# Optimization experiments

Hardware: AMD Instinct MI355X
Metric: run time of the kernel (lower is better)

## Reference

```python
import jax, jax.numpy as jnp
import numpy as np

B, IMG, CIN, COUT = 8, 256, 64, 64
TILE_NUM, KSIZE = 4, 5
TILE = IMG // TILE_NUM                 # 64
FFT = KSIZE + TILE - 1                 # 68
PAD = (FFT - TILE) // 2                # 2


def setup_inputs() -> dict:
    key = jax.random.key(0)
    kx, kk = jax.random.split(key)
    x = jax.random.normal(kx, (B, IMG, IMG, CIN), dtype=jnp.float32)
    # build(): spatial random kernel -> fft2d -> trainable real/imag parts
    kernel_init = jax.random.normal(kk, (COUT, CIN, FFT, FFT), dtype=jnp.float32)
    kernel_fft = jnp.fft.fft2(kernel_init.astype(jnp.complex64))
    kernel_real = jnp.real(kernel_fft).astype(jnp.float32)
    kernel_imag = jnp.imag(kernel_fft).astype(jnp.float32)
    bias = jnp.zeros((COUT,), dtype=jnp.float32)
    return {"x": x, "kernel_real": kernel_real, "kernel_imag": kernel_imag, "bias": bias}


def _stitch(parts, pad, axis):
    """Overlap-add concat of tiles along `axis` with `pad` overlapping pixels."""
    parts = [jnp.moveaxis(p, axis, -1) for p in parts]
    out = parts[0]
    for p in parts[1:]:
        out = jnp.concatenate(
            [out[..., :-pad], out[..., -pad:] + p[..., :pad], p[..., pad:]], axis=-1)
    return jnp.moveaxis(out, -1, axis)


def reference(x, kernel_real, kernel_imag, bias):
    # x: [B, H, W, Cin] NHWC. Extract non-overlapping TILE x TILE tiles
    # (extract_glimpse centered at tile centers == plain tiling).
    b = x.shape[0]
    tiles = x.reshape(b, TILE_NUM, TILE, TILE_NUM, TILE, CIN)
    tiles = tiles.transpose(0, 1, 3, 5, 2, 4)            # [B, tr, tc, Cin, T, T]
    # pad_to_bounding_box: place tile at (PAD, PAD) inside FFT x FFT canvas
    tiles = jnp.pad(tiles, ((0, 0), (0, 0), (0, 0), (0, 0), (PAD, PAD), (PAD, PAD)))
    tiles_fft = jnp.fft.fft2(tiles.astype(jnp.complex64))  # [B, tr, tc, Cin, F, F]
    kfreq = jax.lax.complex(kernel_real, kernel_imag)      # [Cout, Cin, F, F]
    # complex multiply + reduce over input channels
    out_fft = jnp.einsum('brcihw,oihw->brcohw', tiles_fft, kfreq)
    out_tiles = jnp.real(jnp.fft.ifft2(out_fft)) + bias[:, None, None]  # [B,tr,tc,Cout,F,F]
    # overlap-add stitch: columns (last axis) then rows (axis -2)
    rows = [_stitch([out_tiles[:, r, c] for c in range(TILE_NUM)], PAD, axis=-1)
            for r in range(TILE_NUM)]
    full = _stitch(rows, PAD, axis=-2)                     # [B, Cout, Hs, Ws]
    full = full.transpose(0, 2, 3, 1)                      # NHWC
    return full[:, :IMG, :IMG, :]                          # crop_to_bounding_box(0,0,IMG,IMG)
```

## Files before the change

### kernel.cpp

```cpp
#include <hip/hip_runtime.h>
#include <hip/hip_bf16.h>


#define KH   35
#define CHS  4874240ull
#define KTB_FLOATS 9748480ull
#define WS_HEAD 34456ull

typedef float f32x4 __attribute__((ext_vector_type(4)));
typedef short s16x8 __attribute__((ext_vector_type(8)));

__device__ __forceinline__ ushort f2bf(float f) {
    __hip_bfloat16 h = __float2bfloat16(f);
    return *reinterpret_cast<ushort*>(&h);
}
__device__ __forceinline__ uint pkbf(float re, float im) {
    return (uint)f2bf(re) | ((uint)f2bf(im) << 16);
}

__global__ void k_twiddle(float* ws) {
    const float TWO_PI = 6.28318530717958647692f;
    int t = threadIdx.x;
    ushort* Wfb = (ushort*)(ws + 13976);
    for (int e = t; e < 80 * 64; e += 256) {
        int k = e >> 6, r = e & 63;
        float vr = 0.f, vi = 0.f;
        if (k < 68) {
            int ph = (k * (r + 2)) % 68;
            float a = TWO_PI * (float)ph / 68.0f;
            vr = cosf(a); vi = -sinf(a);
        }
        Wfb[e]        = f2bf(vr);
        Wfb[5120 + e] = f2bf(vi);
    }
    ushort* Wib = (ushort*)(ws + 19096);
    for (int e = t; e < 80 * 96; e += 256) {
        int p = e / 96, k = e % 96;
        float vr = 0.f, vi = 0.f;
        if (p < 68 && k < 68) {
            int ph = (p * k) % 68;
            float a = TWO_PI * (float)ph / 68.0f;
            vr = cosf(a) / 68.0f; vi = sinf(a) / 68.0f;
        }
        int dst = p * 128 + (((k >> 3) ^ (p & 7)) << 3) + (k & 7);
        Wib[dst]         = f2bf(vr);
        Wib[10240 + dst] = f2bf(vi);
    }
    ushort* Wgb = (ushort*)(ws + 29336);
    for (int e = t; e < 80 * 96; e += 256) {
        int q = e / 96, k = e % 96;
        float v = 0.f;
        if (q < 68 && k < 70) {
            int k2 = (k < KH) ? k : (k - KH);
            int ph = (q * k2) % 68;
            float a = TWO_PI * (float)ph / 68.0f;
            float alpha = (k2 == 0 || k2 == 34) ? 1.0f : 2.0f;
            v = (k < KH) ? (alpha * cosf(a) / 68.0f)
                         : (-alpha * sinf(a) / 68.0f);
        }
        int dst = q * 128 + (((k >> 3) ^ (q & 7)) << 3) + (k & 7);
        Wgb[dst] = f2bf(v);
    }
}

__global__ void k_zero_seams(float* out) {
    int b = blockIdx.x / 12, line = blockIdx.x % 12;
    const int seam[6] = {66, 67, 132, 133, 198, 199};
    int t = threadIdx.x;
    if (line < 6) {
        int y = seam[line];
        float4* dst = (float4*)(out + ((size_t)(b * 256 + y)) * 256 * 64);
        for (int e = t; e < 4096; e += 256) dst[e] = make_float4(0, 0, 0, 0);
    } else {
        int x = seam[line - 6];
        float4* dst = (float4*)out;
        for (int e = t; e < 4096; e += 256) {
            int y = e >> 4, f = e & 15;
            dst[(((size_t)(b * 256 + y)) * 256 + x) * 16 + f] = make_float4(0, 0, 0, 0);
        }
    }
}

__global__ void k_ktrans(const float* __restrict__ kr, const float* __restrict__ ki,
                         float* __restrict__ Kt) {
    __shared__ float tr[64 * 37];
    __shared__ float ti[64 * 37];
    int k1 = blockIdx.x >> 6, i = blockIdx.x & 63;
    int t = threadIdx.x;
    for (int e = t; e < 64 * KH; e += 256) {
        int o = e / KH, k2 = e % KH;
        size_t src = ((size_t)(o * 64 + i) * 68 + k1) * 68 + k2;
        tr[o * 37 + k2] = kr[src];
        ti[o * 37 + k2] = ki[src];
    }
    __syncthreads();
    for (int e = t; e < KH * 64; e += 256) {
        int k2 = e >> 6, o = e & 63;
        size_t dst = ((size_t)(k1 * KH + k2)) * 8192 + (size_t)i * 128 + o * 2;
        Kt[dst]     = tr[o * 37 + k2];
        Kt[dst + 1] = ti[o * 37 + k2];
    }
}

__global__ void k_kconv(const float* __restrict__ Kt, ushort* __restrict__ Ktb) {
    __shared__ float kl[64 * 130];
    int bin = blockIdx.x;
    int t = threadIdx.x;
    const float4* src = (const float4*)(Kt + (size_t)bin * 8192);
    for (int e = t; e < 2048; e += 256) {
        float4 v = src[e];
        int i = e >> 5, oc = (e & 31) << 2;
        kl[i * 130 + oc]     = v.x;
        kl[i * 130 + oc + 1] = v.y;
        kl[i * 130 + oc + 2] = v.z;
        kl[i * 130 + oc + 3] = v.w;
    }
    __syncthreads();
    ushort* dst = Ktb + (size_t)bin * 8192;
    for (int e = t; e < 4096; e += 256) {
        int o = e >> 6, i = e & 63;
        int sw = (o << 6) + (((i >> 3) ^ (o & 7)) << 3) + (i & 7);
        dst[sw]        = f2bf(kl[i * 130 + 2 * o]);
        dst[4096 + sw] = f2bf(kl[i * 130 + 2 * o + 1]);
    }
}

__global__ __launch_bounds__(512) void k_fwd_row(
        const float* __restrict__ x, const ushort* __restrict__ Wfb,
        uint* __restrict__ Y, int c0) {
    __shared__ __align__(16) ushort sAr[48 * 64];
    __shared__ __align__(16) ushort sAi[48 * 64];
    __shared__ __align__(16) ushort sB[4 * 64 * 64];
    int gid = blockIdx.x;
    int lc = gid >> 8;
    int rem = gid & 255;
    int nl = rem >> 4, rq = rem & 15;
    int n = (c0 + lc) * 16 + nl;
    int b = n >> 4, tr = (n >> 2) & 3, tc = n & 3;
    int t = threadIdx.x;
    for (int e = t; e < 3072; e += 512) {
        int m = e >> 6, c = e & 63;
        int sw = (m << 6) + (((c >> 3) ^ (m & 7)) << 3) + (c & 7);
        sAr[sw] = Wfb[e];
        sAi[sw] = Wfb[5120 + e];
    }
    for (int e = t; e < 4096; e += 512) {
        int rr = e >> 10, f = e & 1023;
        int c = f >> 4, i0 = (f & 15) << 2;
        int y = tr * 64 + rq * 4 + rr;
        const float4* src = (const float4*)(x + ((size_t)(b * 256 + y) * 256
                                                 + tc * 64) * 64 + (c << 6) + i0);
        float4 v = *src;
        float vv[4] = {v.x, v.y, v.z, v.w};
        #pragma unroll
        for (int u = 0; u < 4; ++u) {
            int i = i0 + u;
            sB[(rr << 12) + (i << 6) + (((c >> 3) ^ (i & 7)) << 3) + (c & 7)]
                = f2bf(vv[u]);
        }
    }
    __syncthreads();
    uint* Yc = Y + (size_t)lc * CHS;
    int lane = t & 63, w = t >> 6;
    int lm = lane & 15, kg = lane >> 4;
    int ba0 = ((kg ^ (lm & 7)) << 3);
    int ba1 = (((kg + 4) ^ (lm & 7)) << 3);
    for (int tid = w; tid < 48; tid += 8) {
        int rr = tid / 12, rem2 = tid % 12;
        int mt = rem2 >> 2, nt = rem2 & 3;
        int am = mt * 16 + lm, bn = nt * 16 + lm;
        s16x8 a0r = *(const s16x8*)(sAr + (am << 6) + ba0);
        s16x8 a1r = *(const s16x8*)(sAr + (am << 6) + ba1);
        s16x8 a0i = *(const s16x8*)(sAi + (am << 6) + ba0);
        s16x8 a1i = *(const s16x8*)(sAi + (am << 6) + ba1);
        s16x8 b0 = *(const s16x8*)(sB + (rr << 12) + (bn << 6) + ba0);
        s16x8 b1 = *(const s16x8*)(sB + (rr << 12) + (bn << 6) + ba1);
        f32x4 yr = {0.f, 0.f, 0.f, 0.f}, yi = yr;
        yr = __builtin_amdgcn_mfma_f32_16x16x32_bf16(a0r, b0, yr, 0, 0, 0);
        yr = __builtin_amdgcn_mfma_f32_16x16x32_bf16(a1r, b1, yr, 0, 0, 0);
        yi = __builtin_amdgcn_mfma_f32_16x16x32_bf16(a0i, b0, yi, 0, 0, 0);
        yi = __builtin_amdgcn_mfma_f32_16x16x32_bf16(a1i, b1, yi, 0, 0, 0);
        int r = rq * 4 + rr;
        #pragma unroll
        for (int g2 = 0; g2 < 4; ++g2) {
            int k2 = mt * 16 + kg * 4 + g2;
            if (k2 < KH)
                Yc[((size_t)(nl * KH + k2) * 64 + r) * 64 + nt * 16 + lm]
                    = pkbf(yr[g2], yi[g2]);
        }
    }
}

__global__ __launch_bounds__(512) void k_fwd_col(
        const uint* __restrict__ Y, const ushort* __restrict__ Wfb,
        uint* __restrict__ X) {
    __shared__ __align__(16) ushort sAr[80 * 64];
    __shared__ __align__(16) ushort sAi[80 * 64];
    __shared__ __align__(16) ushort sBr[64 * 64];
    __shared__ __align__(16) ushort sBi[64 * 64];
    int lc = blockIdx.x / 560;
    int rem = blockIdx.x % 560;
    int nl = rem / KH, k2 = rem % KH;
    const uint* Yg = Y + (size_t)lc * CHS + ((size_t)(nl * KH + k2)) * 4096;
    uint* Xc = X + (size_t)lc * CHS;
    int t = threadIdx.x;
    for (int e = t; e < 5120; e += 512) {
        int m = e >> 6, r = e & 63;
        int sw = (m << 6) + ((((r >> 3) ^ (m & 7))) << 3) + (r & 7);
        sAr[sw] = Wfb[e];
        sAi[sw] = Wfb[5120 + e];
    }
    for (int e = t; e < 4096; e += 512) {
        int i = e & 63, r = e >> 6;
        uint v = Yg[e];
        int sw = (i << 6) + ((((r >> 3) ^ (i & 7))) << 3) + (r & 7);
        sBr[sw] = (ushort)(v & 0xffff);
        sBi[sw] = (ushort)(v >> 16);
    }
    __syncthreads();
    int lane = t & 63, w = t >> 6;
    int lm = lane & 15, kg = lane >> 4;
    int ba0 = ((kg ^ (lm & 7)) << 3);
    int ba1 = (((kg + 4) ^ (lm & 7)) << 3);
    for (int tid = w; tid < 20; tid += 8) {
        int mt = tid >> 2, nt = tid & 3;
        int am = mt * 16 + lm, bn = nt * 16 + lm;
        s16x8 ar0 = *(const s16x8*)(sAr + (am << 6) + ba0);
        s16x8 ar1 = *(const s16x8*)(sAr + (am << 6) + ba1);
        s16x8 ai0 = *(const s16x8*)(sAi + (am << 6) + ba0);
        s16x8 ai1 = *(const s16x8*)(sAi + (am << 6) + ba1);
        s16x8 br0 = *(const s16x8*)(sBr + (bn << 6) + ba0);
        s16x8 br1 = *(const s16x8*)(sBr + (bn << 6) + ba1);
        s16x8 bi0 = *(const s16x8*)(sBi + (bn << 6) + ba0);
        s16x8 bi1 = *(const s16x8*)(sBi + (bn << 6) + ba1);
        f32x4 rr = {0.f, 0.f, 0.f, 0.f}, ii = rr, ri = rr, ir = rr;
        rr = __builtin_amdgcn_mfma_f32_16x16x32_bf16(ar0, br0, rr, 0, 0, 0);
        rr = __builtin_amdgcn_mfma_f32_16x16x32_bf16(ar1, br1, rr, 0, 0, 0);
        ii = __builtin_amdgcn_mfma_f32_16x16x32_bf16(ai0, bi0, ii, 0, 0, 0);
        ii = __builtin_amdgcn_mfma_f32_16x16x32_bf16(ai1, bi1, ii, 0, 0, 0);
        ri = __builtin_amdgcn_mfma_f32_16x16x32_bf16(ar0, bi0, ri, 0, 0, 0);
        ri = __builtin_amdgcn_mfma_f32_16x16x32_bf16(ar1, bi1, ri, 0, 0, 0);
        ir = __builtin_amdgcn_mfma_f32_16x16x32_bf16(ai0, br0, ir, 0, 0, 0);
        ir = __builtin_amdgcn_mfma_f32_16x16x32_bf16(ai1, br1, ir, 0, 0, 0);
        #pragma unroll
        for (int g2 = 0; g2 < 4; ++g2) {
            int k1 = mt * 16 + kg * 4 + g2;
            if (k1 < 68)
                Xc[((size_t)(nl * 68 + k1) * KH + k2) * 64 + nt * 16 + lm]
                    = pkbf(rr[g2] - ii[g2], ri[g2] + ir[g2]);
        }
    }
}

__global__ __launch_bounds__(256) void k_mix(
        const uint* __restrict__ X, const ushort* __restrict__ Ktb,
        uint* __restrict__ O) {
    __shared__ __align__(16) ushort sAr[16 * 64];
    __shared__ __align__(16) ushort sAi[16 * 64];
    __shared__ __align__(16) ushort sB[2 * 64 * 64];
    int lc = blockIdx.x / 2380;
    int bin = blockIdx.x % 2380;
    int k1 = bin / KH, k2 = bin % KH;
    const uint* Xc = X + (size_t)lc * CHS;
    uint* Oc = O + (size_t)lc * CHS;
    int t = threadIdx.x;
    for (int e = t; e < 1024; e += 256) {
        int n = e >> 6, i = e & 63;
        uint v = Xc[((size_t)(n * 68 + k1) * KH + k2) * 64 + i];
        int sw = (n << 6) + (((i >> 3) ^ (n & 7)) << 3) + (i & 7);
        sAr[sw] = (ushort)(v & 0xffff);
        sAi[sw] = (ushort)(v >> 16);
    }
    const uint4* ksrc = (const uint4*)(Ktb + (size_t)bin * 8192);
    for (int e = t; e < 1024; e += 256) ((uint4*)sB)[e] = ksrc[e];
    __syncthreads();
    const ushort* sBr = sB;
    const ushort* sBi = sB + 4096;
    int lane = t & 63, w = t >> 6;
    int lm = lane & 15, kg = lane >> 4;
    f32x4 rr = {0.f, 0.f, 0.f, 0.f}, ii = rr, ri = rr, ir = rr;
    #pragma unroll
    for (int st = 0; st < 2; ++st) {
        int blk = kg + st * 4;
        int ao = (lm << 6) + ((blk ^ (lm & 7)) << 3);
        int bo = ((w * 16 + lm) << 6) + ((blk ^ (lm & 7)) << 3);
        s16x8 axr = *(const s16x8*)(sAr + ao);
        s16x8 axi = *(const s16x8*)(sAi + ao);
        s16x8 bxr = *(const s16x8*)(sBr + bo);
        s16x8 bxi = *(const s16x8*)(sBi + bo);
        rr = __builtin_amdgcn_mfma_f32_16x16x32_bf16(axr, bxr, rr, 0, 0, 0);
        ii = __builtin_amdgcn_mfma_f32_16x16x32_bf16(axi, bxi, ii, 0, 0, 0);
        ri = __builtin_amdgcn_mfma_f32_16x16x32_bf16(axr, bxi, ri, 0, 0, 0);
        ir = __builtin_amdgcn_mfma_f32_16x16x32_bf16(axi, bxr, ir, 0, 0, 0);
    }
    #pragma unroll
    for (int g2 = 0; g2 < 4; ++g2) {
        int n = kg * 4 + g2;
        int o = w * 16 + lm;
        Oc[(((size_t)n * KH + k2) * 68 + k1) * 64 + o]
            = pkbf(rr[g2] - ii[g2], ri[g2] + ir[g2]);
    }
}

__global__ __launch_bounds__(512) void k_inv_col(
        const uint* __restrict__ O, const ushort* __restrict__ Wib,
        uint* __restrict__ Z) {
    __shared__ __align__(16) ushort sAr[80 * 128];
    __shared__ __align__(16) ushort sAi[80 * 128];
    __shared__ __align__(16) ushort sBr[64 * 128];
    __shared__ __align__(16) ushort sBi[64 * 128];
    int lc = blockIdx.x / 560;
    int rem = blockIdx.x % 560;
    int nl = rem / KH, k2 = rem % KH;
    int t = threadIdx.x;
    const uint* Ob = O + (size_t)lc * CHS + ((size_t)nl * KH + k2) * 68 * 64;
    uint* Zc = Z + (size_t)lc * CHS;
    const uint4* wsrc = (const uint4*)Wib;
    for (int e = t; e < 1280; e += 512) ((uint4*)sAr)[e] = wsrc[e];
    for (int e = t; e < 1280; e += 512) ((uint4*)sAi)[e] = wsrc[1280 + e];
    uint4 zz = {0, 0, 0, 0};
    for (int e = t; e < 1024; e += 512) { ((uint4*)sBr)[e] = zz; ((uint4*)sBi)[e] = zz; }
    __syncthreads();
    for (int e = t; e < 4352; e += 512) {
        int k1 = e >> 6, o = e & 63;
        uint v = Ob[e];
        int sw = o * 128 + (((k1 >> 3) ^ (o & 7)) << 3) + (k1 & 7);
        sBr[sw] = (ushort)(v & 0xffff);
        sBi[sw] = (ushort)(v >> 16);
    }
    __syncthreads();
    int lane = t & 63, w = t >> 6;
    int lm = lane & 15, kg = lane >> 4;
    for (int tid = w; tid < 20; tid += 8) {
        int mt = tid >> 2, nt = tid & 3;
        int am = mt * 16 + lm, bn = nt * 16 + lm;
        f32x4 rr = {0.f, 0.f, 0.f, 0.f}, ii = rr, ri = rr, ir = rr;
        #pragma unroll
        for (int st = 0; st < 3; ++st) {
            int blk = kg + st * 4;
            int off = ((blk ^ (lm & 7)) << 3);
            s16x8 axr = *(const s16x8*)(sAr + am * 128 + off);
            s16x8 axi = *(const s16x8*)(sAi + am * 128 + off);
            s16x8 bxr = *(const s16x8*)(sBr + bn * 128 + off);
            s16x8 bxi = *(const s16x8*)(sBi + bn * 128 + off);
            rr = __builtin_amdgcn_mfma_f32_16x16x32_bf16(axr, bxr, rr, 0, 0, 0);
            ii = __builtin_amdgcn_mfma_f32_16x16x32_bf16(axi, bxi, ii, 0, 0, 0);
            ri = __builtin_amdgcn_mfma_f32_16x16x32_bf16(axr, bxi, ri, 0, 0, 0);
            ir = __builtin_amdgcn_mfma_f32_16x16x32_bf16(axi, bxr, ir, 0, 0, 0);
        }
        #pragma unroll
        for (int g2 = 0; g2 < 4; ++g2) {
            int p = mt * 16 + kg * 4 + g2;
            if (p < 68)
                Zc[(((size_t)(nl * 68 + p)) * KH + k2) * 64 + nt * 16 + lm]
                    = pkbf(rr[g2] - ii[g2], ri[g2] + ir[g2]);
        }
    }
}

__global__ __launch_bounds__(512) void k_fused_inv(
        const uint* __restrict__ Z, const ushort* __restrict__ Wgb,
        const float* __restrict__ bias, float* __restrict__ out, int c0) {
    __shared__ __align__(16) ushort sWg[80 * 128];
    __shared__ __align__(16) ushort sBq[64 * 128];
    int lc = blockIdx.x / 1088;
    int rem = blockIdx.x % 1088;
    int nl = rem / 68, p = rem % 68;
    int b = c0 + lc;
    int tr = nl >> 2, tc = nl & 3;
    int y = 66 * tr + p;
    if (y >= 256) return;
    int t = threadIdx.x;
    const uint* Zb = Z + (size_t)lc * CHS + ((size_t)(nl * 68 + p)) * KH * 64;
    const uint4* wsrc = (const uint4*)Wgb;
    for (int e = t; e < 1280; e += 512) ((uint4*)sWg)[e] = wsrc[e];
    uint4 zz = {0, 0, 0, 0};
    for (int e = t; e < 1024; e += 512) ((uint4*)sBq)[e] = zz;
    __syncthreads();
    for (int e = t; e < KH * 64; e += 512) {
        int k2 = e >> 6, o = e & 63;
        uint v = Zb[e];
        int kb = k2 + KH;
        sBq[o * 128 + (((k2 >> 3) ^ (o & 7)) << 3) + (k2 & 7)] = (ushort)(v & 0xffff);
        sBq[o * 128 + (((kb >> 3) ^ (o & 7)) << 3) + (kb & 7)] = (ushort)(v >> 16);
    }
    __syncthreads();
    int lane = t & 63, w = t >> 6;
    int lm = lane & 15, kg = lane >> 4;
    bool rowu = !((p <= 1 && tr > 0) || (p >= 66 && tr < 3));
    float* orow = out + ((size_t)(b * 256 + y)) * 256 * 64;
    for (int tid = w; tid < 20; tid += 8) {
        int mt = tid >> 2, nt = tid & 3;
        int am = mt * 16 + lm, bn = nt * 16 + lm;
        f32x4 acc = {0.f, 0.f, 0.f, 0.f};
        #pragma unroll
        for (int st = 0; st < 3; ++st) {
            int blk = kg + st * 4;
            int off = ((blk ^ (lm & 7)) << 3);
            s16x8 av = *(const s16x8*)(sWg + am * 128 + off);
            s16x8 bv = *(const s16x8*)(sBq + bn * 128 + off);
            acc = __builtin_amdgcn_mfma_f32_16x16x32_bf16(av, bv, acc, 0, 0, 0);
        }
        int o = nt * 16 + lm;
        float bv = bias[o];
        #pragma unroll
        for (int g2 = 0; g2 < 4; ++g2) {
            int q = mt * 16 + kg * 4 + g2;
            if (q >= 68) continue;
            int xx = 66 * tc + q;
            if (xx >= 256) continue;
            bool colu = !((q <= 1 && tc > 0) || (q >= 66 && tc < 3));
            float v = acc[g2] + bv;
            float* addr = orow + (size_t)xx * 64 + o;
            if (rowu && colu) *addr = v;
            else              atomicAdd(addr, v);
        }
    }
}

extern "C" void kernel_launch(void* const* d_in, const int* in_sizes, int n_in,
                              void* d_out, int out_size, void* d_ws, size_t ws_size,
                              hipStream_t stream) {
    const float* x    = (const float*)d_in[0];
    const float* kr   = (const float*)d_in[1];
    const float* ki   = (const float*)d_in[2];
    const float* bias = (const float*)d_in[3];
    float* out = (float*)d_out;
    float* ws  = (float*)d_ws;

    int CH = 8;
    while (CH > 4 && (WS_HEAD + KTB_FLOATS + 2ull * CH * CHS) * 4ull > ws_size)
        CH >>= 1;

    ushort* Wfb  = (ushort*)(ws + 13976);
    ushort* Wib  = (ushort*)(ws + 19096);
    ushort* Wgb  = (ushort*)(ws + 29336);
    ushort* Ktb  = (ushort*)(ws + WS_HEAD);
    float*  bufA = ws + WS_HEAD + KTB_FLOATS;
    float*  bufB = bufA + (size_t)CH * CHS;

    k_twiddle<<<1, 256, 0, stream>>>(ws);
    k_ktrans<<<68 * 64, 256, 0, stream>>>(kr, ki, bufB);
    k_kconv<<<2380, 256, 0, stream>>>(bufB, Ktb);
    k_zero_seams<<<96, 256, 0, stream>>>(out);

    for (int s = 0; s < 8; s += CH) {
        k_fwd_row<<<CH * 256, 512, 0, stream>>>(x, Wfb, (uint*)bufA, s);
        k_fwd_col<<<CH * 560, 512, 0, stream>>>((const uint*)bufA, Wfb, (uint*)bufB);
        k_mix<<<CH * 2380, 256, 0, stream>>>((const uint*)bufB, Ktb, (uint*)bufA);
        k_inv_col<<<CH * 560, 512, 0, stream>>>((const uint*)bufA, Wib, (uint*)bufB);
        k_fused_inv<<<CH * 1088, 512, 0, stream>>>((const uint*)bufB, Wgb, bias, out, s);
    }
}
```

Baseline: 414.9 us.

## Fuse kernel prep into one pass and batch four rows per inverse block

Merges the two kernel-weight preprocessing kernels (transpose to fp32 scratch, then bf16 swizzle) into a single kernel that reads kernel_real/imag straight into shared memory and writes the swizzled bf16 layout. This removes the intermediate fp32 round trip through global memory and one launch. The final inverse kernel now handles four output rows per block with double-buffered B tiles, amortising the twiddle-matrix shared-memory load and the bias loads across rows. Fewer blocks are launched in exchange, and each block does more serial work.

Result: faster. 399.6 us (-3.7%).

```diff
diff --git a/kernel.cpp b/kernel.cpp
--- a/kernel.cpp
+++ b/kernel.cpp
@@ -81,47 +81,30 @@
     }
 }
 
-__global__ void k_ktrans(const float* __restrict__ kr, const float* __restrict__ ki,
-                         float* __restrict__ Kt) {
-    __shared__ float tr[64 * 37];
-    __shared__ float ti[64 * 37];
-    int k1 = blockIdx.x >> 6, i = blockIdx.x & 63;
-    int t = threadIdx.x;
-    for (int e = t; e < 64 * KH; e += 256) {
-        int o = e / KH, k2 = e % KH;
-        size_t src = ((size_t)(o * 64 + i) * 68 + k1) * 68 + k2;
-        tr[o * 37 + k2] = kr[src];
-        ti[o * 37 + k2] = ki[src];
-    }
-    __syncthreads();
-    for (int e = t; e < KH * 64; e += 256) {
-        int k2 = e >> 6, o = e & 63;
-        size_t dst = ((size_t)(k1 * KH + k2)) * 8192 + (size_t)i * 128 + o * 2;
-        Kt[dst]     = tr[o * 37 + k2];
-        Kt[dst + 1] = ti[o * 37 + k2];
-    }
-}
-
-__global__ void k_kconv(const float* __restrict__ Kt, ushort* __restrict__ Ktb) {
-    __shared__ float kl[64 * 130];
-    int bin = blockIdx.x;
-    int t = threadIdx.x;
-    const float4* src = (const float4*)(Kt + (size_t)bin * 8192);
-    for (int e = t; e < 2048; e += 256) {
-        float4 v = src[e];
-        int i = e >> 5, oc = (e & 31) << 2;
-        kl[i * 130 + oc]     = v.x;
-        kl[i * 130 + oc + 1] = v.y;
-        kl[i * 130 + oc + 2] = v.z;
-        kl[i * 130 + oc + 3] = v.w;
-    }
-    __syncthreads();
-    ushort* dst = Ktb + (size_t)bin * 8192;
-    for (int e = t; e < 4096; e += 256) {
-        int o = e >> 6, i = e & 63;
-        int sw = (o << 6) + (((i >> 3) ^ (o & 7)) << 3) + (i & 7);
-        dst[sw]        = f2bf(kl[i * 130 + 2 * o]);
-        dst[4096 + sw] = f2bf(kl[i * 130 + 2 * o + 1]);
+__global__ __launch_bounds__(256) void k_kprep(
+        const float* __restrict__ kr, const float* __restrict__ ki,
+        ushort* __restrict__ Ktb) {
+    __shared__ float tr[4 * 64 * KH];
+    __shared__ float ti[4 * 64 * KH];
+    int k1 = blockIdx.x >> 4, oq = blockIdx.x & 15;
+    int t = threadIdx.x;
+    int op = t >> 6, i = t & 63;
+    int o = oq * 4 + op;
+    const float* srcR = kr + ((size_t)(o * 64 + i) * 68 + k1) * 68;
+    const float* srcI = ki + ((size_t)(o * 64 + i) * 68 + k1) * 68;
+    float* tR = tr + (op * 64 + i) * KH;
+    float* tI = ti + (op * 64 + i) * KH;
+    #pragma unroll 7
+    for (int k2 = 0; k2 < KH; ++k2) { tR[k2] = srcR[k2]; tI[k2] = srcI[k2]; }
+    __syncthreads();
+    for (int e = t; e < KH * 256; e += 256) {
+        int k2 = e >> 8, rem = e & 255;
+        int op2 = rem >> 6, i2 = rem & 63;
+        int o2 = oq * 4 + op2;
+        int sw = (((i2 >> 3) ^ (o2 & 7)) << 3) + (i2 & 7);
+        size_t base = ((size_t)(k1 * KH + k2)) * 8192 + (size_t)o2 * 64 + sw;
+        Ktb[base]        = f2bf(tr[(op2 * 64 + i2) * KH + k2]);
+        Ktb[base + 4096] = f2bf(ti[(op2 * 64 + i2) * KH + k2]);
     }
 }
 
@@ -362,58 +345,65 @@
         const uint* __restrict__ Z, const ushort* __restrict__ Wgb,
         const float* __restrict__ bias, float* __restrict__ out, int c0) {
     __shared__ __align__(16) ushort sWg[80 * 128];
-    __shared__ __align__(16) ushort sBq[64 * 128];
-    int lc = blockIdx.x / 1088;
-    int rem = blockIdx.x % 1088;
-    int nl = rem / 68, p = rem % 68;
+    __shared__ __align__(16) ushort sBq[2][64 * 128];
+    int bid = blockIdx.x;
+    int lc = bid / 272;
+    int rem = bid % 272;
+    int nl = rem / 17, pq = rem % 17;
     int b = c0 + lc;
     int tr = nl >> 2, tc = nl & 3;
-    int y = 66 * tr + p;
-    if (y >= 256) return;
-    int t = threadIdx.x;
-    const uint* Zb = Z + (size_t)lc * CHS + ((size_t)(nl * 68 + p)) * KH * 64;
+    int t = threadIdx.x;
     const uint4* wsrc = (const uint4*)Wgb;
     for (int e = t; e < 1280; e += 512) ((uint4*)sWg)[e] = wsrc[e];
     uint4 zz = {0, 0, 0, 0};
-    for (int e = t; e < 1024; e += 512) ((uint4*)sBq)[e] = zz;
-    __syncthreads();
-    for (int e = t; e < KH * 64; e += 512) {
-        int k2 = e >> 6, o = e & 63;
-        uint v = Zb[e];
-        int kb = k2 + KH;
-        sBq[o * 128 + (((k2 >> 3) ^ (o & 7)) << 3) + (k2 & 7)] = (ushort)(v & 0xffff);
-        sBq[o * 128 + (((kb >> 3) ^ (o & 7)) << 3) + (kb & 7)] = (ushort)(v >> 16);
-    }
-    __syncthreads();
+    for (int e = t; e < 2048; e += 512) ((uint4*)sBq[0])[e] = zz;
     int lane = t & 63, w = t >> 6;
     int lm = lane & 15, kg = lane >> 4;
-    bool rowu = !((p <= 1 && tr > 0) || (p >= 66 && tr < 3));
-    float* orow = out + ((size_t)(b * 256 + y)) * 256 * 64;
-    for (int tid = w; tid < 20; tid += 8) {
-        int mt = tid >> 2, nt = tid & 3;
-        int am = mt * 16 + lm, bn = nt * 16 + lm;
-        f32x4 acc = {0.f, 0.f, 0.f, 0.f};
-        #pragma unroll
-        for (int st = 0; st < 3; ++st) {
-            int blk = kg + st * 4;
-            int off = ((blk ^ (lm & 7)) << 3);
-            s16x8 av = *(const s16x8*)(sWg + am * 128 + off);
-            s16x8 bv = *(const s16x8*)(sBq + bn * 128 + off);
-            acc = __builtin_amdgcn_mfma_f32_16x16x32_bf16(av, bv, acc, 0, 0, 0);
-        }
-        int o = nt * 16 + lm;
-        float bv = bias[o];
-        #pragma unroll
-        for (int g2 = 0; g2 < 4; ++g2) {
-            int q = mt * 16 + kg * 4 + g2;
-            if (q >= 68) continue;
-            int xx = 66 * tc + q;
-            if (xx >= 256) continue;
-            bool colu = !((q <= 1 && tc > 0) || (q >= 66 && tc < 3));
-            float v = acc[g2] + bv;
-            float* addr = orow + (size_t)xx * 64 + o;
-            if (rowu && colu) *addr = v;
-            else              atomicAdd(addr, v);
+    float bv4[4];
+    #pragma unroll
+    for (int nt = 0; nt < 4; ++nt) bv4[nt] = bias[nt * 16 + lm];
+    __syncthreads();
+    for (int pp = 0; pp < 4; ++pp) {
+        int p = pq * 4 + pp;
+        int y = 66 * tr + p;
+        if (y >= 256) break;
+        ushort* Bq = sBq[pp & 1];
+        const uint* Zb = Z + (size_t)lc * CHS + ((size_t)(nl * 68 + p)) * KH * 64;
+        for (int e = t; e < KH * 64; e += 512) {
+            int k2 = e >> 6, o = e & 63;
+            uint v = Zb[e];
+            int kb = k2 + KH;
+            Bq[o * 128 + (((k2 >> 3) ^ (o & 7)) << 3) + (k2 & 7)] = (ushort)(v & 0xffff);
+            Bq[o * 128 + (((kb >> 3) ^ (o & 7)) << 3) + (kb & 7)] = (ushort)(v >> 16);
+        }
+        __syncthreads();
+        bool rowu = !((p <= 1 && tr > 0) || (p >= 66 && tr < 3));
+        float* orow = out + ((size_t)(b * 256 + y)) * 256 * 64;
+        for (int tid = w; tid < 20; tid += 8) {
+            int mt = tid >> 2, nt = tid & 3;
+            int am = mt * 16 + lm, bn = nt * 16 + lm;
+            f32x4 acc = {0.f, 0.f, 0.f, 0.f};
+            #pragma unroll
+            for (int st = 0; st < 3; ++st) {
+                int blk = kg + st * 4;
+                int off = ((blk ^ (lm & 7)) << 3);
+                s16x8 av = *(const s16x8*)(sWg + am * 128 + off);
+                s16x8 bv = *(const s16x8*)(Bq + bn * 128 + off);
+                acc = __builtin_amdgcn_mfma_f32_16x16x32_bf16(av, bv, acc, 0, 0, 0);
+            }
+            int o = nt * 16 + lm;
+            #pragma unroll
+            for (int g2 = 0; g2 < 4; ++g2) {
+                int q = mt * 16 + kg * 4 + g2;
+                if (q >= 68) continue;
+                int xx = 66 * tc + q;
+                if (xx >= 256) continue;
+                bool colu = !((q <= 1 && tc > 0) || (q >= 66 && tc < 3));
+                float v = acc[g2] + bv4[nt];
+                float* addr = orow + (size_t)xx * 64 + o;
+                if (rowu && colu) *addr = v;
+                else              atomicAdd(addr, v);
+            }
         }
     }
 }
@@ -440,8 +430,7 @@
     float*  bufB = bufA + (size_t)CH * CHS;
 
     k_twiddle<<<1, 256, 0, stream>>>(ws);
-    k_ktrans<<<68 * 64, 256, 0, stream>>>(kr, ki, bufB);
-    k_kconv<<<2380, 256, 0, stream>>>(bufB, Ktb);
+    k_kprep<<<68 * 16, 256, 0, stream>>>(kr, ki, Ktb);
     k_zero_seams<<<96, 256, 0, stream>>>(out);
 
     for (int s = 0; s < 8; s += CH) {
@@ -449,6 +438,6 @@
         k_fwd_col<<<CH * 560, 512, 0, stream>>>((const uint*)bufA, Wfb, (uint*)bufB);
         k_mix<<<CH * 2380, 256, 0, stream>>>((const uint*)bufB, Ktb, (uint*)bufA);
         k_inv_col<<<CH * 560, 512, 0, stream>>>((const uint*)bufA, Wib, (uint*)bufB);
-        k_fused_inv<<<CH * 1088, 512, 0, stream>>>((const uint*)bufB, Wgb, bias, out, s);
-    }
-}
+        k_fused_inv<<<CH * 272, 512, 0, stream>>>((const uint*)bufB, Wgb, bias, out, s);
+    }
+}
```
